# Kernel tuning notes

Hardware: AMD Instinct MI355X
Metric: run time of the kernel (lower is better)

## Reference

```python
import jax, jax.numpy as jnp
import numpy as np

B, M_IN, H, W = 8, 63, 480, 640
VALID_FRAC = 0.05  # sparse-depth valid pixel density
N_ITERS = 5


def setup_inputs() -> dict:
    key = jax.random.key(0)
    k1, k2, k3 = jax.random.split(key, 3)
    bases = jax.random.normal(k1, (B, M_IN, H, W), dtype=jnp.float32)
    logit = jax.random.normal(k2, (B, 1, H, W), dtype=jnp.float32)
    valid = jax.random.uniform(k3, (B, 1, H, W)) < VALID_FRAC
    # invalid sparse-depth pixels -> log(0) = -inf, ignored via isfinite mask
    targets = jnp.where(valid, logit, -jnp.inf)
    return {"bases": bases, "targets": targets}


def _fit_single(basis, target):
    # basis: (m,h,w), target: (1,h,w)
    m = basis.shape[0]
    y = target[0]                                   # (h,w)
    mask = jnp.isfinite(y)
    maskf = mask.astype(basis.dtype)
    Xf = (basis * maskf).reshape(m, -1)             # masked basis, (m, hw)
    yf = jnp.where(mask, y, 0.0).reshape(-1)        # (hw,)
    XtX = Xf @ Xf.T                                 # (m,m) over valid pixels only
    Xty = Xf @ yf                                   # (m,)
    N = maskf.sum()

    # eval-mode EM-like refinement (prior.use == False): Tr_d = M / beta
    beta0 = jnp.sqrt(N)
    beta = beta0
    done = jnp.array(False)
    for _ in range(N_ITERS):
        w = jnp.linalg.solve(XtX * beta, Xty * beta)    # LU solve
        E_d = jnp.sum((yf - w @ Xf) ** 2)               # residual on valid pixels
        Tr_d = m / beta
        beta_new = N / (E_d + Tr_d)
        conv = jnp.abs(beta_new / beta0 - 1.0) < 0.02
        beta = jnp.where(done, beta, beta_new)
        beta0 = jnp.where(done, beta0, beta_new)
        done = done | conv

    A = XtX * beta
    w = jnp.linalg.solve(A, Xty * beta)                 # (m,)

    # recon3d: predicted log depth
    logit_pred = jnp.einsum('m,mhw->hw', w, basis)[None]  # (1,h,w)

    # pred_var: S_inv via Cholesky, var = (S_inv @ bt * bt).sum(0)
    L = jnp.linalg.cholesky(A)
    S_inv = jax.scipy.linalg.cho_solve((L, True), jnp.eye(m, dtype=basis.dtype))
    bt = basis.reshape(m, -1)                           # (m, hw)
    var = jnp.sum((S_inv @ bt) * bt, axis=0).reshape(1, basis.shape[1], basis.shape[2])
    return logit_pred, w, var


def reference(bases, targets):
    # th_homogenize(append=False): prepend a constant ones basis channel
    ones = jnp.ones_like(bases[:, :1])
    basis_h = jnp.concatenate([ones, bases], axis=1)    # (b, m+1, h, w)
    logits, weights, logit_var = jax.vmap(_fit_single)(basis_h, targets)
    return logits, weights, logit_var
```

## Files before the change

### kernel.cpp

```cpp
#include <hip/hip_runtime.h>
#include <cmath>

#define HW 307200
#define NB 8
#define NBASE 63
#define NCHUNK (HW/256)
#define GRAM_BLKS 128
#define GQCAP 24

#define XTY_OFF 0
#define YTY_OFF (NB*64)
#define NC_OFF  (YTY_OFF + NB)
#define ZERO_FLOATS (NC_OFF + NB)
#define XTX_OFF ZERO_FLOATS
#define MP_OFF  (XTX_OFF + NB*64*64)
#define WV_OFF  (MP_OFF + NB*64*64)

#define OUT_W   (NB*HW)
#define OUT_VAR (OUT_W + NB*64)

__device__ __forceinline__ bool finitef(float x) {
    return (__float_as_uint(x) & 0x7f800000u) != 0x7f800000u;
}

__global__ __launch_bounds__(256) void gram_kernel(
    const float* __restrict__ bases, const float* __restrict__ targets,
    float* __restrict__ ws, float* __restrict__ part)
{
    __shared__ float tile[64*68];
    __shared__ float sy[64];
    __shared__ float sm[64];
    __shared__ int   qg[GQCAP];
    __shared__ int   qmsk[GQCAP];
    __shared__ int   qn;

    const int t  = threadIdx.x;
    const int b  = blockIdx.y;
    const int wv = t >> 6;
    const int l  = t & 63;
    const int ti = l >> 3, tj = l & 7;

    float acc[8][8];
#pragma unroll
    for (int i = 0; i < 8; i++)
#pragma unroll
        for (int j = 0; j < 8; j++) acc[i][j] = 0.f;
    float acc_xty = 0.f, acc_yty = 0.f, acc_n = 0.f;

    const float* __restrict__ basesb = bases + (long)b * NBASE * HW;
    const float* __restrict__ targb  = targets + (long)b * HW;

    if (t == 0) qn = 0;
    __syncthreads();

    auto compute_tile = [&]() {
#pragma unroll 2
        for (int pp = 0; pp < 16; ++pp) {
            const int p2 = wv * 16 + pp;
            const float4 r0 = *(const float4*)&tile[p2*68 + 8*ti];
            const float4 r1 = *(const float4*)&tile[p2*68 + 8*ti + 4];
            const float4 c0 = *(const float4*)&tile[p2*68 + 8*tj];
            const float4 c1 = *(const float4*)&tile[p2*68 + 8*tj + 4];
            const float rr[8] = {r0.x,r0.y,r0.z,r0.w,r1.x,r1.y,r1.z,r1.w};
            const float cc[8] = {c0.x,c0.y,c0.z,c0.w,c1.x,c1.y,c1.z,c1.w};
#pragma unroll
            for (int i = 0; i < 8; i++)
#pragma unroll
                for (int j = 0; j < 8; j++)
                    acc[i][j] = fmaf(rr[i], cc[j], acc[i][j]);
            acc_xty = fmaf(sy[p2], tile[p2*68 + l], acc_xty);
        }
    };

    auto gather_group = [&](int gi) {
        const int pl  = l & 15;
        const int ch4 = l >> 4;
        const float mf = sm[wv*16 + pl];
        const float* __restrict__ gp = basesb + (long)gi * 16 + pl;
#pragma unroll
        for (int q = 0; q < 16; q++) {
            const int c = q*4 + ch4;
            float v;
            if (c == 0) v = mf;
            else        v = gp[(long)(c - 1) * HW] * mf;
            tile[(wv*16 + pl)*68 + c] = v;
        }
    };
    auto zero_group_rows = [&]() {
        const int pl  = l & 15;
        const int ch4 = l >> 4;
#pragma unroll
        for (int q = 0; q < 16; q++)
            tile[(wv*16 + pl)*68 + q*4 + ch4] = 0.f;
    };

    for (int j = blockIdx.x; j < NCHUNK; j += GRAM_BLKS) {
        const int p = j * 256 + t;
        const float y = targb[p];
        const bool fin = finitef(y);
        if (fin) { acc_yty = fmaf(y, y, acc_yty); acc_n += 1.f; }
        const unsigned long long m = __ballot(fin);
        if ((l & 15) == 0) {
            const unsigned gm = (unsigned)((m >> l) & 0xFFFFull);
            if (gm) {
                const int pos = atomicAdd(&qn, 1);
                qg[pos]   = p >> 4;
                qmsk[pos] = (int)gm;
            }
        }
        __syncthreads();
        int nq = qn;
        while (nq >= 4) {
            const int base = nq - 4;
            if (t < 64) {
                const int gsel = t >> 4;
                const int gi   = qg[base + gsel];
                const int msk  = qmsk[base + gsel];
                const int pix  = gi*16 + (t & 15);
                const float yv = targb[pix];
                const bool v   = (msk >> (t & 15)) & 1;
                sm[t] = v ? 1.f : 0.f;
                sy[t] = v ? yv : 0.f;
            }
            __syncthreads();
            gather_group(qg[base + wv]);
            __syncthreads();
            compute_tile();
            nq = base;
            __syncthreads();
        }
        if (t == 0) qn = nq;
        __syncthreads();
    }

    {
        const int nq = qn;
        if (nq > 0) {
            if (t < 64) {
                const int gsel = t >> 4;
                if (gsel < nq) {
                    const int gi  = qg[gsel];
                    const int msk = qmsk[gsel];
                    const int pix = gi*16 + (t & 15);
                    const float yv = targb[pix];
                    const bool v   = (msk >> (t & 15)) & 1;
                    sm[t] = v ? 1.f : 0.f;
                    sy[t] = v ? yv : 0.f;
                } else { sm[t] = 0.f; sy[t] = 0.f; }
            }
            __syncthreads();
            if (wv < nq) gather_group(qg[wv]);
            else         zero_group_rows();
            __syncthreads();
            compute_tile();
        }
    }
    __syncthreads();

    for (int w = 0; w < 4; ++w) {
        if (wv == w) {
#pragma unroll
            for (int i = 0; i < 8; i++)
#pragma unroll
                for (int j2 = 0; j2 < 8; j2++) {
                    const int e = (8*ti + i) * 64 + 8*tj + j2;
                    tile[e] = (w == 0) ? acc[i][j2] : tile[e] + acc[i][j2];
                }
        }
        __syncthreads();
    }
    float* __restrict__ pb = part + (long)(b * GRAM_BLKS + blockIdx.x) * 4096;
#pragma unroll
    for (int k = 0; k < 4; ++k)
        *(float4*)&pb[t*16 + 4*k] = *(const float4*)&tile[t*16 + 4*k];

    for (int w = 0; w < 4; ++w) {
        if (wv == w) tile[4096 + l] = (w == 0) ? acc_xty : tile[4096 + l] + acc_xty;
        __syncthreads();
    }
    if (t < 64) atomicAdd(&ws[XTY_OFF + b*64 + t], tile[4096 + t]);

#pragma unroll
    for (int off = 32; off; off >>= 1) {
        acc_yty += __shfl_down(acc_yty, off, 64);
        acc_n   += __shfl_down(acc_n,   off, 64);
    }
    if (l == 0) {
        atomicAdd(&ws[YTY_OFF + b], acc_yty);
        atomicAdd(&ws[NC_OFF  + b], acc_n);
    }
}

__global__ __launch_bounds__(256) void reduce_kernel(
    const float* __restrict__ part, float* __restrict__ ws)
{
    const int b = blockIdx.y;
    const int e = blockIdx.x * 256 + threadIdx.x;
    const float* __restrict__ pb = part + (long)b * GRAM_BLKS * 4096 + e;
    float s = 0.f;
#pragma unroll 8
    for (int k = 0; k < GRAM_BLKS; ++k)
        s += pb[(long)k * 4096];
    ws[XTX_OFF + b*4096 + e] = s;
}

__global__ __launch_bounds__(64) void solve_kernel(
    float* __restrict__ ws, float* __restrict__ out)
{
    __shared__ float A[64*65];
    __shared__ float d0[64], dinv_s[64], xty_s[64], wv_s[64];

    const int b = blockIdx.x;
    const int t = threadIdx.x;
    const float* XtX = ws + XTX_OFF + b * 4096;

    for (int e = t; e < 4096; e += 64)
        A[(e >> 6) * 65 + (e & 63)] = XtX[e];
    xty_s[t] = ws[XTY_OFF + b*64 + t];
    const float yty = ws[YTY_OFF + b];
    const float Nc  = ws[NC_OFF  + b];
    __syncthreads();
    d0[t] = A[t*65 + t];
    __syncthreads();

    for (int k = 0; k < 64; k++) {
        const float akk = A[k*65 + k];
        __syncthreads();
        const float dk = sqrtf(akk);
        if (t == k)      A[k*65 + k] = dk;
        else if (t > k)  A[t*65 + k] /= dk;
        __syncthreads();
        if (t > k) {
            const float ltk = A[t*65 + k];
            for (int j = k + 1; j <= t; j++)
                A[t*65 + j] -= ltk * A[j*65 + k];
        }
        __syncthreads();
    }

    dinv_s[t] = 1.f / A[t*65 + t];
    __syncthreads();

    float Wc[64];
#pragma unroll
    for (int i = 0; i < 64; i++) {
        float s0 = (i == t) ? 1.f : 0.f, s1 = 0.f, s2 = 0.f, s3 = 0.f;
        const int nfull = i >> 2;
#pragma unroll
        for (int qd = 0; qd < nfull; qd++) {
            const int j = qd * 4;
            s0 = fmaf(-A[i*65 + j    ], Wc[j    ], s0);
            s1 = fmaf(-A[i*65 + j + 1], Wc[j + 1], s1);
            s2 = fmaf(-A[i*65 + j + 2], Wc[j + 2], s2);
            s3 = fmaf(-A[i*65 + j + 3], Wc[j + 3], s3);
        }
#pragma unroll
        for (int j = nfull * 4; j < i; j++)
            s0 = fmaf(-A[i*65 + j], Wc[j], s0);
        Wc[i] = ((s0 + s1) + (s2 + s3)) * dinv_s[i];
    }
#pragma unroll
    for (int i = 63; i >= 0; i--) {
        float s0 = Wc[i], s1 = 0.f, s2 = 0.f, s3 = 0.f;
        const int j0 = i + 1;
        const int nfull = (64 - j0) >> 2;
#pragma unroll
        for (int qd = 0; qd < nfull; qd++) {
            const int j = j0 + qd * 4;
            s0 = fmaf(-A[(j    )*65 + i], Wc[j    ], s0);
            s1 = fmaf(-A[(j + 1)*65 + i], Wc[j + 1], s1);
            s2 = fmaf(-A[(j + 2)*65 + i], Wc[j + 2], s2);
            s3 = fmaf(-A[(j + 3)*65 + i], Wc[j + 3], s3);
        }
#pragma unroll
        for (int j = j0 + nfull * 4; j < 64; j++)
            s0 = fmaf(-A[j*65 + i], Wc[j], s0);
        Wc[i] = ((s0 + s1) + (s2 + s3)) * dinv_s[i];
    }

    float w0 = 0.f, w1 = 0.f, w2 = 0.f, w3 = 0.f;
#pragma unroll
    for (int j = 0; j < 64; j += 4) {
        w0 = fmaf(Wc[j    ], xty_s[j    ], w0);
        w1 = fmaf(Wc[j + 1], xty_s[j + 1], w1);
        w2 = fmaf(Wc[j + 2], xty_s[j + 2], w2);
        w3 = fmaf(Wc[j + 3], xty_s[j + 3], w3);
    }
    const float wt = (w0 + w1) + (w2 + w3);
    wv_s[t] = wt;
    __syncthreads();

    float qt = 0.f;
#pragma unroll
    for (int j = 0; j < 64; j++) {
        const float x = (j > t) ? A[t*65 + j] : ((j == t) ? d0[t] : A[j*65 + t]);
        qt = fmaf(x, wv_s[j], qt);
    }
    float r1 = wt * xty_s[t];
    float r2 = wt * qt;
#pragma unroll
    for (int off = 32; off; off >>= 1) {
        r1 += __shfl_down(r1, off, 64);
        r2 += __shfl_down(r2, off, 64);
    }
    r1 = __shfl(r1, 0, 64);
    r2 = __shfl(r2, 0, 64);
    const float E_d = yty - 2.f * r1 + r2;

    float beta0 = sqrtf(Nc);
    float beta  = beta0;
    bool  done  = false;
#pragma unroll
    for (int it = 0; it < 5; ++it) {
        const float Tr_d = 64.f / beta;
        const float beta_new = Nc / (E_d + Tr_d);
        const bool conv = fabsf(beta_new / beta0 - 1.f) < 0.02f;
        if (!done) { beta = beta_new; beta0 = beta_new; }
        done = done || conv;
    }
    const float ib = 1.f / beta;

    out[OUT_W + b*64 + t] = wt;
    ws[WV_OFF + b*64 + t] = wt;
    float* __restrict__ Mp = ws + MP_OFF + b * 4096;
#pragma unroll
    for (int j = 0; j < 64; j++) {
        const float v = (j > t) ? 0.f : ((j == t) ? 0.5f : 1.f) * Wc[j] * ib;
        Mp[j*64 + t] = v;
    }
}

__global__ __launch_bounds__(256, 2) void predvar_kernel(
    const float* __restrict__ bases, const float* __restrict__ ws,
    float* __restrict__ out)
{
    __shared__ float Mp_s[4096];
    __shared__ float w_s[64];

    const int b = blockIdx.y;
    const int t = threadIdx.x;
    {
        const float4* __restrict__ src = (const float4*)(ws + MP_OFF + b * 4096);
        float4* dst = (float4*)Mp_s;
        for (int e = t; e < 1024; e += 256) dst[e] = src[e];
        if (t < 64) w_s[t] = ws[WV_OFF + b*64 + t];
    }
    __syncthreads();

    const int pix = (blockIdx.x * 256 + t) * 2;
    const float* basesb = bases + (long)b * NBASE * HW + pix;

    float2 bv[64];
    bv[0] = make_float2(1.f, 1.f);
#pragma unroll
    for (int c = 1; c < 64; c++)
        bv[c] = *(const float2*)&basesb[(long)(c - 1) * HW];

    float px = w_s[0], py = w_s[0];
#pragma unroll
    for (int c = 1; c < 64; c++) {
        px = fmaf(w_s[c], bv[c].x, px);
        py = fmaf(w_s[c], bv[c].y, py);
    }

    float vx = 0.f, vy = 0.f;
#pragma unroll
    for (int i = 0; i < 64; i++) {
        float sx = 0.f, sy2 = 0.f;
#pragma unroll
        for (int qd = i >> 2; qd < 16; qd++) {
            const float4 m = *(const float4*)&Mp_s[i*64 + 4*qd];
            sx  = fmaf(m.x, bv[4*qd+0].x, sx);
            sy2 = fmaf(m.x, bv[4*qd+0].y, sy2);
            sx  = fmaf(m.y, bv[4*qd+1].x, sx);
            sy2 = fmaf(m.y, bv[4*qd+1].y, sy2);
            sx  = fmaf(m.z, bv[4*qd+2].x, sx);
            sy2 = fmaf(m.z, bv[4*qd+2].y, sy2);
            sx  = fmaf(m.w, bv[4*qd+3].x, sx);
            sy2 = fmaf(m.w, bv[4*qd+3].y, sy2);
        }
        vx = fmaf(sx,  bv[i].x, vx);
        vy = fmaf(sy2, bv[i].y, vy);
    }

    *(float2*)&out[(long)b * HW + pix] = make_float2(px, py);
    *(float2*)&out[OUT_VAR + (long)b * HW + pix] = make_float2(2.f * vx, 2.f * vy);
}

extern "C" void kernel_launch(void* const* d_in, const int* in_sizes, int n_in,
                              void* d_out, int out_size, void* d_ws, size_t ws_size,
                              hipStream_t stream)
{
    const float* bases   = (const float*)d_in[0];
    const float* targets = (const float*)d_in[1];
    float* out = (float*)d_out;
    float* ws  = (float*)d_ws;

    hipMemsetAsync(d_ws, 0, ZERO_FLOATS * sizeof(float), stream);

    gram_kernel<<<dim3(GRAM_BLKS, NB), 256, 0, stream>>>(bases, targets, ws, out);
    reduce_kernel<<<dim3(16, NB), 256, 0, stream>>>(out, ws);
    solve_kernel<<<NB, 64, 0, stream>>>(ws, out);
    predvar_kernel<<<dim3(HW / 512, NB), 256, 0, stream>>>(bases, ws, out);
}
```

Before: 621.4 us.

## Compact valid pixels per-pixel into dense Gram tiles instead of 16-pixel groups

Replaces the queue of 16-pixel groups, which padded invalid pixels with zeros, with a per-pixel prefix-sum compaction. Only valid pixels are written into a rolling 64-row tile, and basis values are gathered with coalesced float4 loads from the chunk. At about 5% valid density most 16-pixel groups held only one valid pixel, so the old tiles were mostly zeros. The change should cut wasted FMA work and scattered gathers, and the grid drops from 128 to 96 blocks per batch. In exchange, every 256-pixel chunk now reads all 63 channels for any window that has a valid pixel, and extra barriers are added.

```diff
diff --git a/kernel.cpp b/kernel.cpp
--- a/kernel.cpp
+++ b/kernel.cpp
@@ -5,8 +5,7 @@
 #define NB 8
 #define NBASE 63
 #define NCHUNK (HW/256)
-#define GRAM_BLKS 128
-#define GQCAP 24
+#define GRAM_BLKS 96
 
 #define XTY_OFF 0
 #define YTY_OFF (NB*64)
@@ -29,16 +28,17 @@
 {
     __shared__ float tile[64*68];
     __shared__ float sy[64];
-    __shared__ float sm[64];
-    __shared__ int   qg[GQCAP];
-    __shared__ int   qmsk[GQCAP];
-    __shared__ int   qn;
+    __shared__ float yv[256];
+    __shared__ int   smap[256];
+    __shared__ int   wcnt[4];
 
     const int t  = threadIdx.x;
     const int b  = blockIdx.y;
     const int wv = t >> 6;
     const int l  = t & 63;
     const int ti = l >> 3, tj = l & 7;
+    const int q  = l;
+    const int cg = wv;
 
     float acc[8][8];
 #pragma unroll
@@ -49,9 +49,6 @@
 
     const float* __restrict__ basesb = bases + (long)b * NBASE * HW;
     const float* __restrict__ targb  = targets + (long)b * HW;
-
-    if (t == 0) qn = 0;
-    __syncthreads();
 
     auto compute_tile = [&]() {
 #pragma unroll 2
@@ -72,88 +69,74 @@
         }
     };
 
-    auto gather_group = [&](int gi) {
-        const int pl  = l & 15;
-        const int ch4 = l >> 4;
-        const float mf = sm[wv*16 + pl];
-        const float* __restrict__ gp = basesb + (long)gi * 16 + pl;
-#pragma unroll
-        for (int q = 0; q < 16; q++) {
-            const int c = q*4 + ch4;
-            float v;
-            if (c == 0) v = mf;
-            else        v = gp[(long)(c - 1) * HW] * mf;
-            tile[(wv*16 + pl)*68 + c] = v;
-        }
-    };
-    auto zero_group_rows = [&]() {
-        const int pl  = l & 15;
-        const int ch4 = l >> 4;
-#pragma unroll
-        for (int q = 0; q < 16; q++)
-            tile[(wv*16 + pl)*68 + q*4 + ch4] = 0.f;
-    };
+    int tilefill = 0;
 
     for (int j = blockIdx.x; j < NCHUNK; j += GRAM_BLKS) {
-        const int p = j * 256 + t;
-        const float y = targb[p];
+        const int pix0 = j * 256;
+        const float y = targb[pix0 + t];
         const bool fin = finitef(y);
         if (fin) { acc_yty = fmaf(y, y, acc_yty); acc_n += 1.f; }
         const unsigned long long m = __ballot(fin);
-        if ((l & 15) == 0) {
-            const unsigned gm = (unsigned)((m >> l) & 0xFFFFull);
-            if (gm) {
-                const int pos = atomicAdd(&qn, 1);
-                qg[pos]   = p >> 4;
-                qmsk[pos] = (int)gm;
-            }
-        }
-        __syncthreads();
-        int nq = qn;
-        while (nq >= 4) {
-            const int base = nq - 4;
-            if (t < 64) {
-                const int gsel = t >> 4;
-                const int gi   = qg[base + gsel];
-                const int msk  = qmsk[base + gsel];
-                const int pix  = gi*16 + (t & 15);
-                const float yv = targb[pix];
-                const bool v   = (msk >> (t & 15)) & 1;
-                sm[t] = v ? 1.f : 0.f;
-                sy[t] = v ? yv : 0.f;
+        if (l == 0) wcnt[wv] = __popcll(m);
+        yv[t] = y;
+        __syncthreads();
+        int pre = tilefill;
+        for (int w2 = 0; w2 < wv; ++w2) pre += wcnt[w2];
+        const int rank = __popcll(m & ((1ull << l) - 1ull));
+        smap[t] = fin ? (pre + rank) : -1;
+        const int vc = wcnt[0] + wcnt[1] + wcnt[2] + wcnt[3];
+        __syncthreads();
+
+        int   sreg[4]; float yreg[4];
+#pragma unroll
+        for (int i = 0; i < 4; i++) {
+            sreg[i] = smap[4*q + i];
+            yreg[i] = yv[4*q + i];
+        }
+
+        const int nwin = (tilefill + vc) >> 6;
+        for (int w = 0; w <= nwin; ++w) {
+            const bool doW = ((sreg[0] >= 0) & ((sreg[0] >> 6) == w)) |
+                             ((sreg[1] >= 0) & ((sreg[1] >> 6) == w)) |
+                             ((sreg[2] >= 0) & ((sreg[2] >> 6) == w)) |
+                             ((sreg[3] >= 0) & ((sreg[3] >> 6) == w));
+            if (doW) {
+#pragma unroll
+                for (int k = 0; k < 16; k++) {
+                    const int cb = cg + 4*k;
+                    float4 v = make_float4(0.f, 0.f, 0.f, 0.f);
+                    if (cb < 63)
+                        v = *(const float4*)&basesb[(long)cb * HW + pix0 + 4*q];
+#pragma unroll
+                    for (int i = 0; i < 4; i++) {
+                        const int s = sreg[i];
+                        if (s >= 0 && (s >> 6) == w) {
+                            const int row = s & 63;
+                            const float vi = (i == 0) ? v.x : (i == 1) ? v.y
+                                           : (i == 2) ? v.z : v.w;
+                            if (cb < 63) {
+                                tile[row*68 + cb + 1] = vi;
+                            } else {
+                                tile[row*68] = 1.f;
+                                sy[row] = yreg[i];
+                            }
+                        }
+                    }
+                }
             }
             __syncthreads();
-            gather_group(qg[base + wv]);
-            __syncthreads();
-            compute_tile();
-            nq = base;
-            __syncthreads();
-        }
-        if (t == 0) qn = nq;
-        __syncthreads();
-    }
-
-    {
-        const int nq = qn;
-        if (nq > 0) {
-            if (t < 64) {
-                const int gsel = t >> 4;
-                if (gsel < nq) {
-                    const int gi  = qg[gsel];
-                    const int msk = qmsk[gsel];
-                    const int pix = gi*16 + (t & 15);
-                    const float yv = targb[pix];
-                    const bool v   = (msk >> (t & 15)) & 1;
-                    sm[t] = v ? 1.f : 0.f;
-                    sy[t] = v ? yv : 0.f;
-                } else { sm[t] = 0.f; sy[t] = 0.f; }
-            }
-            __syncthreads();
-            if (wv < nq) gather_group(qg[wv]);
-            else         zero_group_rows();
-            __syncthreads();
-            compute_tile();
-        }
+            if (w < nwin) { compute_tile(); __syncthreads(); }
+        }
+        tilefill = (tilefill + vc) & 63;
+    }
+
+    if (tilefill > 0) {
+        for (int r = tilefill + wv; r < 64; r += 4) {
+            tile[r*68 + l] = 0.f;
+            if (l == 0) sy[r] = 0.f;
+        }
+        __syncthreads();
+        compute_tile();
     }
     __syncthreads();
 
```

After: 754.7 us. 21.5% more time.
